# Optimization experiments

Hardware: AMD Instinct MI355X
Metric: run time of the kernel (lower is better)

The kernel has to match this reference:

```python
import jax, jax.numpy as jnp
import numpy as np

B, H, W, C = 16, 64, 80, 256
GH, GW = 8, 10            # grid partition_size
HEADS, DH = 8, 32         # C // dim_head heads
INNER = 1024              # int(4 * C), gated=False MLP
SCALE = DH ** -0.5
EPS = 1e-5


def _layernorm(x, g, b):
    m = jnp.mean(x, axis=-1, keepdims=True)
    v = jnp.mean(jnp.square(x - m), axis=-1, keepdims=True)
    return (x - m) * jax.lax.rsqrt(v + EPS) * g + b


def setup_inputs() -> dict:
    key = jax.random.key(0)
    ks = jax.random.split(key, 12)
    s = 0.02
    return {
        "x": jax.random.normal(ks[0], (B, H, W, C), jnp.float32),
        "norm1_g": jnp.ones((C,), jnp.float32),
        "norm1_b": jnp.zeros((C,), jnp.float32),
        "qkv_w": jax.random.normal(ks[1], (C, 3 * C), jnp.float32) * s,
        "qkv_b": jnp.zeros((3 * C,), jnp.float32),
        "proj_w": jax.random.normal(ks[2], (C, C), jnp.float32) * s,
        "proj_b": jnp.zeros((C,), jnp.float32),
        "ls1_g": jnp.full((C,), 1e-5, jnp.float32),
        "norm2_g": jnp.ones((C,), jnp.float32),
        "norm2_b": jnp.zeros((C,), jnp.float32),
        "fc1_w": jax.random.normal(ks[3], (C, INNER), jnp.float32) * s,
        "fc1_b": jnp.zeros((INNER,), jnp.float32),
        "fc2_w": jax.random.normal(ks[4], (INNER, C), jnp.float32) * s,
        "fc2_b": jnp.zeros((C,), jnp.float32),
        "ls2_g": jnp.full((C,), 1e-5, jnp.float32),
    }


def _grid_partition(x):
    # [B,H,W,C] -> [B*(H/GH)*(W/GW), GH*GW, C] (GRID: strided/dilated windows)
    x = x.reshape(B, GH, H // GH, GW, W // GW, C)
    x = x.transpose(0, 2, 4, 1, 3, 5)
    return x.reshape(-1, GH * GW, C)


def _grid_reverse(w):
    x = w.reshape(B, H // GH, W // GW, GH, GW, C)
    x = x.transpose(0, 3, 1, 4, 2, 5)
    return x.reshape(B, H, W, C)


def _self_attn(p, qkv_w, qkv_b, proj_w, proj_b):
    nW, N, _ = p.shape
    qkv = p @ qkv_w + qkv_b                         # [nW, N, 3C]
    qkv = qkv.reshape(nW, N, HEADS, 3 * DH).transpose(0, 2, 1, 3)
    q, k, v = jnp.split(qkv, 3, axis=-1)            # each [nW, heads, N, DH]
    attn = jnp.einsum('whnd,whmd->whnm', q, k) * SCALE
    attn = jax.nn.softmax(attn, axis=-1)
    o = jnp.einsum('whnm,whmd->whnd', attn, v)
    o = o.transpose(0, 2, 1, 3).reshape(nW, N, C)
    return o @ proj_w + proj_b


def reference(x, norm1_g, norm1_b, qkv_w, qkv_b, proj_w, proj_b, ls1_g,
              norm2_g, norm2_b, fc1_w, fc1_b, fc2_w, fc2_b, ls2_g):
    # --- partition attention branch ---
    h = _layernorm(x, norm1_g, norm1_b)
    p = _grid_partition(h)
    p = _self_attn(p, qkv_w, qkv_b, proj_w, proj_b)
    attn_out = _grid_reverse(p)
    x = x + ls1_g * attn_out
    # --- MLP branch (gated=False: Linear -> GELU -> Linear) ---
    h = _layernorm(x, norm2_g, norm2_b)
    h = jax.nn.gelu(h @ fc1_w + fc1_b, approximate=False)
    h = h @ fc2_w + fc2_b
    return x + ls2_g * h
```

## Files before the change

kernel.cpp:

```cpp
#include <hip/hip_runtime.h>
#include <hip/hip_bf16.h>
#include <stdint.h>
#include <math.h>

typedef __bf16 bf16_t;
typedef __bf16 bf16x8 __attribute__((ext_vector_type(8)));
typedef __bf16 bf16x4 __attribute__((ext_vector_type(4)));
typedef float  f32x4  __attribute__((ext_vector_type(4)));
typedef long long i64_t;

typedef __attribute__((address_space(1))) const void global_cv;
typedef __attribute__((address_space(3))) void lds_v;


__device__ __forceinline__ int map_p_to_g(int p) {
    int w = p / 80, n = p - w * 80;
    int b  = w >> 6, h2 = (w >> 3) & 7, w2 = w & 7;
    int gh = n / 10, gw = n - gh * 10;
    return b * 5120 + (gh * 8 + h2) * 80 + (gw * 8 + w2);
}

__device__ __forceinline__ int swz128(int b) { return b ^ (((b >> 7) & 7) << 4); }

__global__ __launch_bounds__(256) void wconv_k(const float* __restrict__ in,
                                               bf16_t* __restrict__ out, int N, int K)
{
    int i = blockIdx.x * 256 + threadIdx.x;
    int n = i / K, k = i - n * K;
    out[i] = (bf16_t)in[(size_t)k * N + n];
}

__global__ __launch_bounds__(256) void wconv8_k(const float* __restrict__ in,
                                                unsigned char* __restrict__ out)
{
    int c  = blockIdx.x * 256 + threadIdx.x;
    int n  = (c * 4) >> 10;
    int k0 = (c * 4) & 1023;
    float g0 = 16.f * in[(size_t)(k0 + 0) * 256 + n];
    float g1 = 16.f * in[(size_t)(k0 + 1) * 256 + n];
    float g2 = 16.f * in[(size_t)(k0 + 2) * 256 + n];
    float g3 = 16.f * in[(size_t)(k0 + 3) * 256 + n];
    int pk = __builtin_amdgcn_cvt_pk_fp8_f32(g0, g1, 0, false);
    pk     = __builtin_amdgcn_cvt_pk_fp8_f32(g2, g3, pk, true);
    *(int*)(out + (size_t)c * 4) = pk;
}

template <int PERM>
__global__ __launch_bounds__(256) void ln_k(const float* __restrict__ in,
                                            const float* __restrict__ gg,
                                            const float* __restrict__ bb,
                                            bf16_t* __restrict__ o)
{
    int row  = blockIdx.x * 4 + (threadIdx.x >> 6);
    int lane = threadIdx.x & 63;
    const float4 xv = *(const float4*)(in + (size_t)row * 256 + lane * 4);
    float s = xv.x + xv.y + xv.z + xv.w;
#pragma unroll
    for (int m = 1; m < 64; m <<= 1) s += __shfl_xor(s, m, 64);
    float mean = s * (1.f / 256.f);
    float d0 = xv.x - mean, d1 = xv.y - mean, d2 = xv.z - mean, d3 = xv.w - mean;
    float v = d0 * d0 + d1 * d1 + d2 * d2 + d3 * d3;
#pragma unroll
    for (int m = 1; m < 64; m <<= 1) v += __shfl_xor(v, m, 64);
    float rstd = rsqrtf(v * (1.f / 256.f) + 1e-5f);
    const float4 gv = *(const float4*)(gg + lane * 4);
    const float4 bv = *(const float4*)(bb + lane * 4);
    int orow = row;
    if (PERM) {
        int b = row / 5120, r1 = row - b * 5120;
        int h = r1 / 80, wv = r1 - h * 80;
        int gh = h >> 3, h2 = h & 7, gw = wv >> 3, w2 = wv & 7;
        orow = ((b * 8 + h2) * 8 + w2) * 80 + gh * 10 + gw;
    }
    bf16x4 ov;
    ov[0] = (bf16_t)(d0 * rstd * gv.x + bv.x);
    ov[1] = (bf16_t)(d1 * rstd * gv.y + bv.y);
    ov[2] = (bf16_t)(d2 * rstd * gv.z + bv.z);
    ov[3] = (bf16_t)(d3 * rstd * gv.w + bv.w);
    *(bf16x4*)(o + (size_t)orow * 256 + lane * 4) = ov;
}

template <int EPI, int NBX>
__device__ __forceinline__ void gemm_body(const bf16_t* __restrict__ A,
                                          const bf16_t* __restrict__ Bt,
                                          const float* __restrict__ bias,
                                          const float* __restrict__ xres,
                                          const float* __restrict__ ls,
                                          void* __restrict__ outp,
                                          int N, int K)
{
    __shared__ bf16_t At[128 * 64];
    __shared__ bf16_t Bl[64 * 64];
    const int t = threadIdx.x;
    const int wid = t >> 6, lane = t & 63;
    const int ln = lane & 15, kg = lane >> 4;

    const int f   = blockIdx.x;
    const int xcd = f & 7, jj = f >> 3;
    const int byx = (gridDim.x >> 3) / NBX;
    const int by  = xcd * byx + jj / NBX;
    const int bx  = jj % NBX;

    const size_t Kb = (size_t)K * 2;
    const char* Ab = (const char*)(A  + (size_t)by * 128 * K);
    const char* Bb = (const char*)(Bt + (size_t)bx * 64 * K);
    char* AtB = (char*)At;
    char* BlB = (char*)Bl;

    int spa[4], sra[4], soa[4];
#pragma unroll
    for (int i = 0; i < 4; ++i) {
        spa[i] = (i * 256 + t) * 16;
        sra[i] = spa[i] >> 7;
        soa[i] = (spa[i] & 127) ^ ((sra[i] & 7) << 4);
    }
    int spb[2], srb[2], sob[2];
#pragma unroll
    for (int i = 0; i < 2; ++i) {
        spb[i] = (i * 256 + t) * 16;
        srb[i] = spb[i] >> 7;
        sob[i] = (spb[i] & 127) ^ ((srb[i] & 7) << 4);
    }

    const f32x4 fz = {0.f, 0.f, 0.f, 0.f};
    f32x4 acc[2][4];
#pragma unroll
    for (int i = 0; i < 2; ++i)
#pragma unroll
        for (int j = 0; j < 4; ++j) acc[i][j] = fz;

    const int nsteps = K >> 6;

    for (int s = 0; s < nsteps; ++s) {
        const size_t kb = (size_t)s * 128;
#pragma unroll
        for (int i = 0; i < 4; ++i)
            __builtin_amdgcn_global_load_lds((global_cv*)(Ab + (size_t)sra[i] * Kb + kb + soa[i]),
                                             (lds_v*)(AtB + spa[i]), 16, 0, 0);
#pragma unroll
        for (int i = 0; i < 2; ++i)
            __builtin_amdgcn_global_load_lds((global_cv*)(Bb + (size_t)srb[i] * Kb + kb + sob[i]),
                                             (lds_v*)(BlB + spb[i]), 16, 0, 0);
        __syncthreads();
#pragma unroll
        for (int kk = 0; kk < 2; ++kk) {
            bf16x8 av[2], bv[4];
#pragma unroll
            for (int mt = 0; mt < 2; ++mt) {
                int row = wid * 32 + mt * 16 + ln;
                av[mt] = *(const bf16x8*)(AtB + swz128(row * 128 + kk * 64 + kg * 16));
            }
#pragma unroll
            for (int nt = 0; nt < 4; ++nt) {
                int row = nt * 16 + ln;
                bv[nt] = *(const bf16x8*)(BlB + swz128(row * 128 + kk * 64 + kg * 16));
            }
#pragma unroll
            for (int mt = 0; mt < 2; ++mt)
#pragma unroll
                for (int nt = 0; nt < 4; ++nt)
                    acc[mt][nt] = __builtin_amdgcn_mfma_f32_16x16x32_bf16(bv[nt], av[mt], acc[mt][nt], 0, 0, 0);
        }
        __syncthreads();
    }

#pragma unroll
    for (int mt = 0; mt < 2; ++mt) {
        const int row = by * 128 + wid * 32 + mt * 16 + ln;
        const int wno = row / 80, tok = row - wno * 80;
#pragma unroll
        for (int nt = 0; nt < 4; ++nt) {
            const int colb = bx * 64 + nt * 16 + kg * 4;
            const f32x4 a = acc[mt][nt];
            const float4 b4 = *(const float4*)(bias + colb);
            if constexpr (EPI == 0) {
                bf16_t* o = (bf16_t*)outp;
                const int typ = colb >> 8, h = (colb >> 5) & 7, d0 = colb & 31;
                const size_t base = (size_t)wno * 61440 + (size_t)h * 7680;
                if (typ < 2) {
                    bf16x4 ov;
                    ov[0] = (bf16_t)(a[0] + b4.x); ov[1] = (bf16_t)(a[1] + b4.y);
                    ov[2] = (bf16_t)(a[2] + b4.z); ov[3] = (bf16_t)(a[3] + b4.w);
                    *(bf16x4*)(o + base + typ * 2560 + tok * 32 + d0) = ov;
                } else {
#pragma unroll
                    for (int r = 0; r < 4; ++r)
                        o[base + 5120 + (size_t)(d0 + r) * 80 + tok] =
                            (bf16_t)(a[r] + ((const float*)&b4)[r]);
                }
            } else if constexpr (EPI == 1) {
                const float4 l4 = *(const float4*)(ls + colb);
                float* o = (float*)outp;
                int g = map_p_to_g(row);
                size_t idx = (size_t)g * 256 + colb;
                float4 xr = *(const float4*)(xres + idx);
                float4 r4;
                r4.x = xr.x + l4.x * (a[0] + b4.x);
                r4.y = xr.y + l4.y * (a[1] + b4.y);
                r4.z = xr.z + l4.z * (a[2] + b4.z);
                r4.w = xr.w + l4.w * (a[3] + b4.w);
                *(float4*)(o + idx) = r4;
            } else {
                unsigned char* o = (unsigned char*)outp;
                float g4[4];
#pragma unroll
                for (int r = 0; r < 4; ++r) {
                    float u2 = a[r] + ((const float*)&b4)[r];
                    float e = __expf(-1.702f * u2);
                    g4[r] = (16.f * u2) * __builtin_amdgcn_rcpf(1.f + e);
                }
                int pk = __builtin_amdgcn_cvt_pk_fp8_f32(g4[0], g4[1], 0, false);
                pk     = __builtin_amdgcn_cvt_pk_fp8_f32(g4[2], g4[3], pk, true);
                *(int*)(o + (size_t)row * N + colb) = pk;
            }
        }
    }
}

__global__ __launch_bounds__(256, 6) void gq_k(const bf16_t* A, const bf16_t* Bt, const float* bias,
                                               void* outp, int N, int K)
{ gemm_body<0, 12>(A, Bt, bias, nullptr, nullptr, outp, N, K); }

__global__ __launch_bounds__(256, 6) void gp_k(const bf16_t* A, const bf16_t* Bt, const float* bias,
                                               const float* xres, const float* ls, void* outp, int N, int K)
{ gemm_body<1, 4>(A, Bt, bias, xres, ls, outp, N, K); }

__global__ __launch_bounds__(256, 6) void g1_k(const bf16_t* A, const bf16_t* Bt, const float* bias,
                                               void* outp, int N, int K)
{ gemm_body<2, 16>(A, Bt, bias, nullptr, nullptr, outp, N, K); }

__global__ __launch_bounds__(256, 4) void g2f8_k(const unsigned char* __restrict__ A,
                                                 const unsigned char* __restrict__ Bt,
                                                 const float* __restrict__ bias,
                                                 const float* __restrict__ ls,
                                                 float* __restrict__ out)
{
    __shared__ __align__(16) char At[8192];
    __shared__ __align__(16) char Bl[8192];
    const int t = threadIdx.x;
    const int wid = t >> 6, lane = t & 63;
    const int wr = wid >> 1, wc = wid & 1;
    const int ln = lane & 15, kg = lane >> 4;

    const int f   = blockIdx.x;
    const int xcd = f & 7, jj = f >> 3;
    const int byx = (gridDim.x >> 3) / 2;
    const int by  = xcd * byx + jj / 2;
    const int bx  = jj & 1;

    const char* Ab = (const char*)A  + (size_t)by * 128 * 1024;
    const char* Bb = (const char*)Bt + (size_t)bx * 128 * 1024;

    const f32x4 fz = {0.f, 0.f, 0.f, 0.f};
    f32x4 acc[4][4];
#pragma unroll
    for (int i = 0; i < 4; ++i)
#pragma unroll
        for (int j = 0; j < 4; ++j) acc[i][j] = fz;

    for (int s = 0; s < 16; ++s) {
        const size_t kb = (size_t)s * 64;
#pragma unroll
        for (int i = 0; i < 2; ++i) {
            int p   = (i * 256 + t) * 16;
            int row = p >> 6;
            int off = (p & 63) ^ ((row & 3) << 4);
            __builtin_amdgcn_global_load_lds((global_cv*)(Ab + (size_t)row * 1024 + kb + off),
                                             (lds_v*)(At + p), 16, 0, 0);
            __builtin_amdgcn_global_load_lds((global_cv*)(Bb + (size_t)row * 1024 + kb + off),
                                             (lds_v*)(Bl + p), 16, 0, 0);
        }
        __syncthreads();
#pragma unroll
        for (int kk = 0; kk < 2; ++kk) {
            i64_t av[4], bv[4];
#pragma unroll
            for (int mt = 0; mt < 4; ++mt) {
                int row = wr * 64 + mt * 16 + ln;
                av[mt] = *(const i64_t*)(At + row * 64 + ((kk * 32 + kg * 8) ^ ((row & 3) << 4)));
            }
#pragma unroll
            for (int nt = 0; nt < 4; ++nt) {
                int row = wc * 64 + nt * 16 + ln;
                bv[nt] = *(const i64_t*)(Bl + row * 64 + ((kk * 32 + kg * 8) ^ ((row & 3) << 4)));
            }
#pragma unroll
            for (int mt = 0; mt < 4; ++mt)
#pragma unroll
                for (int nt = 0; nt < 4; ++nt)
                    acc[mt][nt] = __builtin_amdgcn_mfma_f32_16x16x32_fp8_fp8(bv[nt], av[mt], acc[mt][nt], 0, 0, 0);
        }
        __syncthreads();
    }

#pragma unroll
    for (int mt = 0; mt < 4; ++mt) {
        const int row = by * 128 + wr * 64 + mt * 16 + ln;
#pragma unroll
        for (int nt = 0; nt < 4; ++nt) {
            const int colb = bx * 128 + wc * 64 + nt * 16 + kg * 4;
            const f32x4 a = acc[mt][nt];
            const float4 b4 = *(const float4*)(bias + colb);
            const float4 l4 = *(const float4*)(ls + colb);
            size_t idx = (size_t)row * 256 + colb;
            float4 cur = *(const float4*)(out + idx);
            cur.x += l4.x * (a[0] * 0.00390625f + b4.x);
            cur.y += l4.y * (a[1] * 0.00390625f + b4.y);
            cur.z += l4.z * (a[2] * 0.00390625f + b4.z);
            cur.w += l4.w * (a[3] * 0.00390625f + b4.w);
            *(float4*)(out + idx) = cur;
        }
    }
}

__global__ __launch_bounds__(256) void attn_k(const bf16_t* __restrict__ qkvt,
                                              bf16_t* __restrict__ out)
{
    __shared__ bf16_t Plds[4 * 2 * 1408];
    const int t = threadIdx.x, wid = t >> 6, lane = t & 63;
    const int ln = lane & 15, kg = lane >> 4;
    bf16_t* P0 = &Plds[wid * 2816];
    bf16_t* P1 = P0 + 1408;
    const int b = blockIdx.x;
    const int w = b >> 1;
    const int h = (b & 1) * 4 + wid;
    const float SCALE = 0.17677669529663689f;

    const bf16_t* Qb = qkvt + (size_t)w * 61440 + (size_t)h * 7680;
    const bf16_t* Kb = Qb + 2560;
    const bf16_t* Vb = Qb + 5120;

    bf16x8 kb[5];
#pragma unroll
    for (int nt = 0; nt < 5; ++nt)
        kb[nt] = *(const bf16x8*)(Kb + (nt * 16 + ln) * 32 + kg * 8);

#pragma unroll
    for (int mt = 0; mt < 5; ++mt) {
        bf16x8 qa = *(const bf16x8*)(Qb + (mt * 16 + ln) * 32 + kg * 8);
        f32x4 S[5];
#pragma unroll
        for (int nt = 0; nt < 5; ++nt) {
            f32x4 z = {0.f, 0.f, 0.f, 0.f};
            S[nt] = __builtin_amdgcn_mfma_f32_16x16x32_bf16(qa, kb[nt], z, 0, 0, 0);
        }
#pragma unroll
        for (int r = 0; r < 4; ++r) {
            float mx = S[0][r];
#pragma unroll
            for (int nt = 1; nt < 5; ++nt) mx = fmaxf(mx, S[nt][r]);
            mx = fmaxf(mx, __shfl_xor(mx, 1, 64));
            mx = fmaxf(mx, __shfl_xor(mx, 2, 64));
            mx = fmaxf(mx, __shfl_xor(mx, 4, 64));
            mx = fmaxf(mx, __shfl_xor(mx, 8, 64));
            float sum = 0.f;
#pragma unroll
            for (int nt = 0; nt < 5; ++nt) {
                float e = __expf((S[nt][r] - mx) * SCALE);
                S[nt][r] = e;
                sum += e;
            }
            sum += __shfl_xor(sum, 1, 64);
            sum += __shfl_xor(sum, 2, 64);
            sum += __shfl_xor(sum, 4, 64);
            sum += __shfl_xor(sum, 8, 64);
            float inv = 1.f / sum;
#pragma unroll
            for (int nt = 0; nt < 5; ++nt) S[nt][r] *= inv;
        }
        bf16_t* Pc = (mt & 1) ? P1 : P0;
#pragma unroll
        for (int nt = 0; nt < 5; ++nt)
#pragma unroll
            for (int r = 0; r < 4; ++r)
                Pc[(kg * 4 + r) * 88 + nt * 16 + ln] = (bf16_t)S[nt][r];
        f32x4 O[2];
        O[0] = (f32x4){0.f, 0.f, 0.f, 0.f};
        O[1] = (f32x4){0.f, 0.f, 0.f, 0.f};
#pragma unroll
        for (int nt2 = 0; nt2 < 2; ++nt2) {
#pragma unroll
            for (int kt = 0; kt < 3; ++kt) {
                const bool dead = (kt == 2) && (kg >= 2);
                int off = kt * 32 + kg * 8;
                if (off >= 80) off = 0;
                bf16x8 bv = *(const bf16x8*)(Vb + (nt2 * 16 + ln) * 80 + off);
                if (dead) {
#pragma unroll
                    for (int j = 0; j < 8; ++j) bv[j] = (bf16_t)0.f;
                }
                int cb = kt * 32 + kg * 8;
                if (cb >= 80) cb = 0;
                bf16x8 av = *(const bf16x8*)(Pc + ln * 88 + cb);
                O[nt2] = __builtin_amdgcn_mfma_f32_16x16x32_bf16(av, bv, O[nt2], 0, 0, 0);
            }
        }
#pragma unroll
        for (int nt2 = 0; nt2 < 2; ++nt2)
#pragma unroll
            for (int r = 0; r < 4; ++r) {
                int n = mt * 16 + kg * 4 + r;
                out[((size_t)w * 80 + n) * 256 + h * 32 + nt2 * 16 + ln] = (bf16_t)O[nt2][r];
            }
    }
}

extern "C" void kernel_launch(void* const* d_in, const int* in_sizes, int n_in,
                              void* d_out, int out_size, void* d_ws, size_t ws_size,
                              hipStream_t stream)
{
    (void)in_sizes; (void)n_in; (void)out_size; (void)ws_size;
    const float* x     = (const float*)d_in[0];
    const float* n1g   = (const float*)d_in[1];
    const float* n1b   = (const float*)d_in[2];
    const float* qkvw  = (const float*)d_in[3];
    const float* qkvb  = (const float*)d_in[4];
    const float* projw = (const float*)d_in[5];
    const float* projb = (const float*)d_in[6];
    const float* ls1   = (const float*)d_in[7];
    const float* n2g   = (const float*)d_in[8];
    const float* n2b   = (const float*)d_in[9];
    const float* fc1w  = (const float*)d_in[10];
    const float* fc1b  = (const float*)d_in[11];
    const float* fc2w  = (const float*)d_in[12];
    const float* fc2b  = (const float*)d_in[13];
    const float* ls2   = (const float*)d_in[14];
    float* out = (float*)d_out;

    char* ws = (char*)d_ws;
    bf16_t* actA   = (bf16_t*)(ws);
    bf16_t* qkvt   = (bf16_t*)(ws + 41943040ull);
    unsigned char* h1f8 = (unsigned char*)(ws + 41943040ull);
    bf16_t* wbuf   = (bf16_t*)(ws + 209715200ull);
    bf16_t* qkvwt  = wbuf;
    bf16_t* projwt = qkvwt + 768 * 256;
    bf16_t* fc1wt  = projwt + 256 * 256;
    unsigned char* fc2w8 = (unsigned char*)(fc1wt + 1024 * 256);

    wconv_k<<<768,  256, 0, stream>>>(qkvw,  qkvwt, 768, 256);
    wconv_k<<<256,  256, 0, stream>>>(projw, projwt, 256, 256);
    wconv_k<<<1024, 256, 0, stream>>>(fc1w,  fc1wt, 1024, 256);
    wconv8_k<<<256, 256, 0, stream>>>(fc2w, fc2w8);

    ln_k<1><<<20480, 256, 0, stream>>>(x, n1g, n1b, actA);
    gq_k<<<7680, 256, 0, stream>>>(actA, qkvwt, qkvb, qkvt, 768, 256);
    attn_k<<<2048, 256, 0, stream>>>(qkvt, actA);
    gp_k<<<2560, 256, 0, stream>>>(actA, projwt, projb, x, ls1, out, 256, 256);
    ln_k<0><<<20480, 256, 0, stream>>>(out, n2g, n2b, actA);
    g1_k<<<10240, 256, 0, stream>>>(actA, fc1wt, fc1b, h1f8, 1024, 256);
    g2f8_k<<<1280, 256, 0, stream>>>(h1f8, fc2w8, fc2b, ls2, out);
}
```

Measured before the change: 385.1 us.

## Store fc1 FP8 output in K-tiled layout and transpose weights via LDS tiles

The fc1 GEMM epilogue now writes its FP8 GELU output in a K-blocked layout: 64-byte column slabs, each holding all rows contiguously. The fc2 GEMM can then load each A tile as one contiguous 8 KB chunk instead of rows strided by 1024 bytes. Separately, the weight-conversion kernel is replaced with a 64x64 shared-memory tiled transpose, so both its reads and writes are coalesced. In exchange, the fc1 epilogue writes at finer granularity, which may scatter its stores, and the intermediate layout is now coupled between the two kernels.

```diff
diff --git a/kernel.cpp b/kernel.cpp
--- a/kernel.cpp
+++ b/kernel.cpp
@@ -22,12 +22,23 @@
 
 __device__ __forceinline__ int swz128(int b) { return b ^ (((b >> 7) & 7) << 4); }
 
-__global__ __launch_bounds__(256) void wconv_k(const float* __restrict__ in,
-                                               bf16_t* __restrict__ out, int N, int K)
-{
-    int i = blockIdx.x * 256 + threadIdx.x;
-    int n = i / K, k = i - n * K;
-    out[i] = (bf16_t)in[(size_t)k * N + n];
+__global__ __launch_bounds__(256) void wconvt_k(const float* __restrict__ in,
+                                                bf16_t* __restrict__ out, int N, int K)
+{
+    __shared__ float tile[64][65];
+    const int n0 = blockIdx.x * 64, k0 = blockIdx.y * 64;
+    const int tn = threadIdx.x & 63, tr = threadIdx.x >> 6;
+#pragma unroll
+    for (int i = 0; i < 16; ++i) {
+        int k = i * 4 + tr;
+        tile[k][tn] = in[(size_t)(k0 + k) * N + n0 + tn];
+    }
+    __syncthreads();
+#pragma unroll
+    for (int i = 0; i < 16; ++i) {
+        int n = i * 4 + tr;
+        out[(size_t)(n0 + n) * K + k0 + tn] = (bf16_t)tile[tn][n];
+    }
 }
 
 __global__ __launch_bounds__(256) void wconv8_k(const float* __restrict__ in,
@@ -211,7 +222,7 @@
                 }
                 int pk = __builtin_amdgcn_cvt_pk_fp8_f32(g4[0], g4[1], 0, false);
                 pk     = __builtin_amdgcn_cvt_pk_fp8_f32(g4[2], g4[3], pk, true);
-                *(int*)(o + (size_t)row * N + colb) = pk;
+                *(int*)(o + (size_t)bx * 5242880 + (size_t)row * 64 + nt * 16 + kg * 4) = pk;
             }
         }
     }
@@ -248,7 +259,7 @@
     const int by  = xcd * byx + jj / 2;
     const int bx  = jj & 1;
 
-    const char* Ab = (const char*)A  + (size_t)by * 128 * 1024;
+    const char* Ab = (const char*)A  + (size_t)by * 8192;
     const char* Bb = (const char*)Bt + (size_t)bx * 128 * 1024;
 
     const f32x4 fz = {0.f, 0.f, 0.f, 0.f};
@@ -260,12 +271,13 @@
 
     for (int s = 0; s < 16; ++s) {
         const size_t kb = (size_t)s * 64;
+        const char* As = Ab + (size_t)s * 5242880;
 #pragma unroll
         for (int i = 0; i < 2; ++i) {
             int p   = (i * 256 + t) * 16;
             int row = p >> 6;
             int off = (p & 63) ^ ((row & 3) << 4);
-            __builtin_amdgcn_global_load_lds((global_cv*)(Ab + (size_t)row * 1024 + kb + off),
+            __builtin_amdgcn_global_load_lds((global_cv*)(As + (size_t)row * 64 + off),
                                              (lds_v*)(At + p), 16, 0, 0);
             __builtin_amdgcn_global_load_lds((global_cv*)(Bb + (size_t)row * 1024 + kb + off),
                                              (lds_v*)(Bl + p), 16, 0, 0);
@@ -430,16 +442,16 @@
     char* ws = (char*)d_ws;
     bf16_t* actA   = (bf16_t*)(ws);
     bf16_t* qkvt   = (bf16_t*)(ws + 41943040ull);
-    unsigned char* h1f8 = (unsigned char*)(ws + 41943040ull);
+    unsigned char* h1t = (unsigned char*)(ws + 41943040ull);
     bf16_t* wbuf   = (bf16_t*)(ws + 209715200ull);
     bf16_t* qkvwt  = wbuf;
     bf16_t* projwt = qkvwt + 768 * 256;
     bf16_t* fc1wt  = projwt + 256 * 256;
     unsigned char* fc2w8 = (unsigned char*)(fc1wt + 1024 * 256);
 
-    wconv_k<<<768,  256, 0, stream>>>(qkvw,  qkvwt, 768, 256);
-    wconv_k<<<256,  256, 0, stream>>>(projw, projwt, 256, 256);
-    wconv_k<<<1024, 256, 0, stream>>>(fc1w,  fc1wt, 1024, 256);
+    wconvt_k<<<dim3(12, 4), 256, 0, stream>>>(qkvw,  qkvwt, 768, 256);
+    wconvt_k<<<dim3(4, 4),  256, 0, stream>>>(projw, projwt, 256, 256);
+    wconvt_k<<<dim3(16, 4), 256, 0, stream>>>(fc1w,  fc1wt, 1024, 256);
     wconv8_k<<<256, 256, 0, stream>>>(fc2w, fc2w8);
 
     ln_k<1><<<20480, 256, 0, stream>>>(x, n1g, n1b, actA);
@@ -447,6 +459,6 @@
     attn_k<<<2048, 256, 0, stream>>>(qkvt, actA);
     gp_k<<<2560, 256, 0, stream>>>(actA, projwt, projb, x, ls1, out, 256, 256);
     ln_k<0><<<20480, 256, 0, stream>>>(out, n2g, n2b, actA);
-    g1_k<<<10240, 256, 0, stream>>>(actA, fc1wt, fc1b, h1f8, 1024, 256);
-    g2f8_k<<<1280, 256, 0, stream>>>(h1f8, fc2w8, fc2b, ls2, out);
-}
+    g1_k<<<10240, 256, 0, stream>>>(actA, fc1wt, fc1b, h1t, 1024, 256);
+    g2f8_k<<<1280, 256, 0, stream>>>(h1t, fc2w8, fc2b, ls2, out);
+}
```

Result: no change. 385.4 us (median of 4 runs) (+0.1%).
